# Performance work log

Measured on AMD Instinct MI355X. Metric: run time of the kernel, lower is better.

## Reference

```python
import jax, jax.numpy as jnp
import numpy as np

E = 8        # n_routed_experts
K = 2        # n_experts_per_token
H = 1024     # d_hidden
D = 512      # d_expert
NSH = 2      # n_shared_experts -> shared expert width = D*NSH


def setup_inputs() -> dict:
    key = jax.random.key(0)
    ks = jax.random.split(key, 8)
    s = 0.02
    x = jax.random.normal(ks[0], (4, 2048, H), jnp.float32)
    W_router = (jax.random.normal(ks[1], (H, E), jnp.float32) * s)
    Wg = (jax.random.normal(ks[2], (E, H, D), jnp.float32) * s)   # per-expert gate proj
    Wu = (jax.random.normal(ks[3], (E, H, D), jnp.float32) * s)   # per-expert up proj
    Wd = (jax.random.normal(ks[4], (E, D, H), jnp.float32) * s)   # per-expert down proj
    Ds = D * NSH
    Wsg = (jax.random.normal(ks[5], (H, Ds), jnp.float32) * s)
    Wsu = (jax.random.normal(ks[6], (H, Ds), jnp.float32) * s)
    Wsd = (jax.random.normal(ks[7], (Ds, H), jnp.float32) * s)
    return {"x": x, "W_router": W_router, "Wg": Wg, "Wu": Wu, "Wd": Wd,
            "Wsg": Wsg, "Wsu": Wsu, "Wsd": Wsd}


def reference(x, W_router, Wg, Wu, Wd, Wsg, Wsu, Wsd):
    B, S, Hd = x.shape
    T = B * S
    xf = x.reshape(T, Hd)

    # shared expert (SwiGLU)
    shared = (jax.nn.silu(xf @ Wsg) * (xf @ Wsu)) @ Wsd          # [T, H]

    # gating: softmax -> top-k -> renormalize
    logits = xf @ W_router                                        # [T, E]
    probs = jax.nn.softmax(logits, axis=-1)
    topk_scores, topk_idx = jax.lax.top_k(probs, K)               # [T, K]
    topk_scores = topk_scores / jnp.sum(topk_scores, axis=-1, keepdims=True)

    # combine weights: zero for unselected experts (topk indices are distinct,
    # so the original's first-match score selection equals a simple scatter)
    combine = jnp.zeros((T, E), x.dtype).at[jnp.arange(T)[:, None], topk_idx].set(topk_scores)

    # per-expert SwiGLU, computed densely and combined with sparse weights
    gate = jax.nn.silu(jnp.einsum('th,ehd->etd', xf, Wg))         # [E, T, D]
    up = jnp.einsum('th,ehd->etd', xf, Wu)                        # [E, T, D]
    expert_out = jnp.einsum('etd,edh->eth', gate * up, Wd)        # [E, T, H]
    routed = jnp.einsum('eth,te->th', expert_out, combine)        # [T, H]

    out = (routed + shared).reshape(B, S, Hd)

    # load-balancing aux loss: E * sum(mean_probs^2)
    probs_mean = jnp.mean(probs.reshape(B, S, E), axis=(0, 1))
    aux_loss = E * jnp.sum(probs_mean * probs_mean)
    return out, aux_loss
```

## Files before the change

### kernel.cpp

```cpp
#include <hip/hip_runtime.h>


typedef unsigned short u16;
typedef unsigned int   u32;
typedef short short8 __attribute__((ext_vector_type(8)));
typedef float f32x4  __attribute__((ext_vector_type(4)));

#define AS1 __attribute__((address_space(1)))
#define AS3 __attribute__((address_space(3)))

constexpr int T  = 8192;
constexpr int H  = 1024;
constexpr int E  = 8;
constexpr int D  = 512;
constexpr int DS = 1024;
constexpr int PAIR_CAP  = 18432;
constexpr int MT_ROUTED = 72;
constexpr int RB = 512;

constexpr int GU_ROUTED_BLKS = 4 * MT_ROUTED;
constexpr int GU_SHARED_BLKS = 8 * (T / 256);
constexpr int GU_BLKS  = GU_ROUTED_BLKS + GU_SHARED_BLKS;
constexpr int DNR_BLKS = 4 * MT_ROUTED;
constexpr int DNS_BLKS = 4 * (T / 256);
constexpr int DN_BLKS  = DNR_BLKS + DNS_BLKS;

__device__ __forceinline__ u16 f2bf(float f){
  u32 u = __builtin_bit_cast(u32, f);
  u += 0x7fffu + ((u >> 16) & 1u);
  return (u16)(u >> 16);
}
__device__ __forceinline__ float bf2f(u16 h){
  u32 u = ((u32)h) << 16;
  return __builtin_bit_cast(float, u);
}

__device__ __forceinline__ void gl_lds16(const u16* g, u16* l){
  __builtin_amdgcn_global_load_lds((const AS1 void*)g, (AS3 void*)l, 16, 0, 0);
}

template<int N>
__device__ __forceinline__ void wait_vm(){ __builtin_amdgcn_s_waitcnt(0x0f70 | N); }

__device__ __forceinline__ void bar_raw(){
  __builtin_amdgcn_s_barrier();
}
__device__ __forceinline__ void bar_pin(){
  __builtin_amdgcn_s_barrier();
  __builtin_amdgcn_sched_barrier(0);
}

__device__ __forceinline__ int swz_off(int c, int lane){
  return ((c ^ (lane & 7)) * 8);
}

template<int NWG>
__device__ __forceinline__ int xcd_tau(int fid){
  return (fid & 7) * (NWG >> 3) + (fid >> 3);
}

__global__ void __launch_bounds__(256) router_kernel(
    const float* __restrict__ x, const float* __restrict__ Wr,
    u16* __restrict__ xb,
    int* __restrict__ topk_idx, float* __restrict__ topk_w,
    int* __restrict__ partial_hist, float* __restrict__ partial_probs)
{
  __shared__ int   hist_s[4][8];
  __shared__ float ps_s[4][8];
  int tid = threadIdx.x, lane = tid & 63, wv = tid >> 6;
  int   histl[8] = {0,0,0,0,0,0,0,0};
  float psl[8]   = {0.f,0.f,0.f,0.f,0.f,0.f,0.f,0.f};

  for (int it = 0; it < 4; ++it){
    int t = blockIdx.x * 16 + wv * 4 + it;
    const float4* xr = (const float4*)(x + (long)t * H);
    uint2* xbr = (uint2*)(xb + (long)t * H);
    float acc[8];
#pragma unroll
    for (int e = 0; e < 8; ++e) acc[e] = 0.f;
#pragma unroll
    for (int i = 0; i < 4; ++i){
      float4 xv = xr[i * 64 + lane];
      u32 lo = (u32)f2bf(xv.x) | ((u32)f2bf(xv.y) << 16);
      u32 hi = (u32)f2bf(xv.z) | ((u32)f2bf(xv.w) << 16);
      xbr[i * 64 + lane] = make_uint2(lo, hi);
      int h0 = i * 256 + lane * 4;
#pragma unroll
      for (int j = 0; j < 4; ++j){
        float xs = (j == 0) ? xv.x : (j == 1) ? xv.y : (j == 2) ? xv.z : xv.w;
        const float4* wr = (const float4*)(Wr + (long)(h0 + j) * E);
        float4 w0 = wr[0], w1 = wr[1];
        acc[0] += xs * w0.x; acc[1] += xs * w0.y; acc[2] += xs * w0.z; acc[3] += xs * w0.w;
        acc[4] += xs * w1.x; acc[5] += xs * w1.y; acc[6] += xs * w1.z; acc[7] += xs * w1.w;
      }
    }
#pragma unroll
    for (int off = 32; off >= 1; off >>= 1){
#pragma unroll
      for (int e = 0; e < 8; ++e) acc[e] += __shfl_xor(acc[e], off, 64);
    }
    if (lane == 0){
      float m = acc[0];
#pragma unroll
      for (int e = 1; e < 8; ++e) m = fmaxf(m, acc[e]);
      float p[8], s = 0.f;
#pragma unroll
      for (int e = 0; e < 8; ++e){ p[e] = __expf(acc[e] - m); s += p[e]; }
      float inv = 1.f / s;
#pragma unroll
      for (int e = 0; e < 8; ++e) psl[e] += p[e] * inv;
      int i1 = 0; float v1 = p[0];
#pragma unroll
      for (int e = 1; e < 8; ++e) if (p[e] > v1){ v1 = p[e]; i1 = e; }
      int i2 = -1; float v2 = -1.f;
#pragma unroll
      for (int e = 0; e < 8; ++e) if (e != i1 && p[e] > v2){ v2 = p[e]; i2 = e; }
      float rs = 1.f / (v1 + v2);
      topk_idx[2 * t] = i1; topk_idx[2 * t + 1] = i2;
      topk_w[2 * t] = v1 * rs; topk_w[2 * t + 1] = v2 * rs;
      histl[i1]++; histl[i2]++;
    }
  }
  if (lane == 0){
#pragma unroll
    for (int e = 0; e < 8; ++e){ hist_s[wv][e] = histl[e]; ps_s[wv][e] = psl[e]; }
  }
  __syncthreads();
  if (tid < 8){
    int hs = 0; float ps = 0.f;
#pragma unroll
    for (int w = 0; w < 4; ++w){ hs += hist_s[w][tid]; ps += ps_s[w][tid]; }
    partial_hist[blockIdx.x * 8 + tid]  = hs;
    partial_probs[blockIdx.x * 8 + tid] = ps;
  }
}

__global__ void __launch_bounds__(64) scan_kernel(
    const int* __restrict__ partial_hist, const float* __restrict__ partial_probs,
    int* __restrict__ block_offset, float* __restrict__ out_aux,
    int* __restrict__ meta)
{
  __shared__ int   csum[8][8];
  __shared__ float cps[8][8];
  __shared__ int   cbase[8][8];
  __shared__ int   base_s[8];
  int tid = threadIdx.x, e = tid & 7, c = tid >> 3;
  int s = 0; float f = 0.f;
  for (int b = c * 64; b < c * 64 + 64; ++b){
    s += partial_hist[b * 8 + e]; f += partial_probs[b * 8 + e];
  }
  csum[c][e] = s; cps[c][e] = f;
  __syncthreads();
  if (tid < 8){
    int tot = 0;
    for (int cc = 0; cc < 8; ++cc){ cbase[cc][tid] = tot; tot += csum[cc][tid]; }
    csum[0][tid] = tot;
  }
  __syncthreads();
  if (tid == 0){
    int off = 0;
    for (int ee = 0; ee < 8; ++ee){ base_s[ee] = off; off += (csum[0][ee] + 255) & ~255; }
    meta[0] = off;
    float a = 0.f;
    for (int ee = 0; ee < 8; ++ee){
      float ps = 0.f;
      for (int cc = 0; cc < 8; ++cc) ps += cps[cc][ee];
      float m = ps * (1.f / (float)T);
      a += m * m;
    }
    out_aux[0] = (float)E * a;
  }
  __syncthreads();
  int run = base_s[e] + cbase[c][e];
  for (int b = c * 64; b < c * 64 + 64; ++b){
    block_offset[b * 8 + e] = run;
    run += partial_hist[b * 8 + e];
  }
}

__global__ void __launch_bounds__(64) scatter_kernel(
    const int* __restrict__ topk_idx, const float* __restrict__ topk_w,
    const int* __restrict__ block_offset,
    int* __restrict__ pair_token, int* __restrict__ pair_expert,
    float* __restrict__ pair_score, int* __restrict__ token_pos)
{
  int lane = threadIdx.x, b = blockIdx.x;
  if (lane >= 32) return;
  int idx = b * 32 + lane;
  int t = idx >> 1;
  int e = topk_idx[idx];
  float w = topk_w[idx];
  unsigned long long below = lane ? ((1ull << lane) - 1ull) : 0ull;
  int rank = 0, basee = 0;
#pragma unroll
  for (int ee = 0; ee < 8; ++ee){
    unsigned long long m = __ballot(e == ee);
    if (e == ee){ rank = __popcll(m & below); basee = block_offset[b * 8 + ee]; }
  }
  int pos = basee + rank;
  pair_token[pos] = t;
  pair_expert[pos] = e;
  pair_score[pos] = w;
  token_pos[idx] = pos;
}

__global__ void __launch_bounds__(256) transpose_all(
    const float* __restrict__ Wsg, const float* __restrict__ Wsu, u16* __restrict__ WsguT,
    const float* __restrict__ Wsd, u16* __restrict__ WsdT,
    const float* __restrict__ Wg,  const float* __restrict__ Wu, u16* __restrict__ WguT,
    const float* __restrict__ Wd,  u16* __restrict__ WdT)
{
  __shared__ float tile[32][33];
  int z = blockIdx.z;
  const float* src; u16* dst; int R, C, itype;
  if (z < 3){
    R = 1024; C = 1024;
    if (z == 0){ src = Wsg; dst = WsguT; itype = 1; }
    else if (z == 1){ src = Wsu; dst = WsguT; itype = 2; }
    else { src = Wsd; dst = WsdT; itype = 0; }
  } else if (z < 19){
    R = 1024; C = 512;
    int p = z - 3;
    if (p < 8){ src = Wg + (long)p * R * C; dst = WguT + (long)p * (2 * D * H); itype = 1; }
    else      { src = Wu + (long)(p - 8) * R * C; dst = WguT + (long)(p - 8) * (2 * D * H); itype = 2; }
  } else {
    R = 512; C = 1024;
    int p = z - 19;
    src = Wd + (long)p * R * C; dst = WdT + (long)p * R * C; itype = 0;
  }
  int tx = threadIdx.x & 31, ty = threadIdx.x >> 5;
  int c = blockIdx.x * 32 + tx;
  int rb = blockIdx.y * 32;
  if (blockIdx.x * 32 >= C || rb >= R) return;
#pragma unroll
  for (int j = 0; j < 4; ++j)
    tile[ty + j * 8][tx] = src[(long)(rb + ty + j * 8) * C + c];
  __syncthreads();
#pragma unroll
  for (int j = 0; j < 4; ++j){
    int cc = blockIdx.x * 32 + ty + j * 8;
    int dr = (itype == 0) ? cc : ((cc >> 4) * 32 + (cc & 15) + ((itype == 2) ? 16 : 0));
    dst[(long)dr * R + rb + tx] = f2bf(tile[tx][ty + j * 8]);
  }
}

struct HalfStage { const u16* p[2]; };

__device__ __forceinline__ void half_init(HalfStage& hs, const u16* __restrict__ gbase,
    int ld, int rowbase, const int* __restrict__ gather, int wave, int lane){
  int lr = lane >> 3, ch = lane & 7;
  int chs = (ch ^ lr) * 8;
#pragma unroll
  for (int j = 0; j < 2; ++j){
    int row = (wave * 2 + j) * 8 + lr;
    int grow = gather ? gather[rowbase + row] : (rowbase + row);
    hs.p[j] = gbase + (long)grow * ld + chs;
  }
}

__device__ __forceinline__ void half_issue(const HalfStage& hs, int k0,
                                           u16* __restrict__ lds, int wave){
#pragma unroll
  for (int j = 0; j < 2; ++j)
    gl_lds16(hs.p[j] + k0, lds + (wave * 2 + j) * 512);
}

template<int EPI>
__device__ __forceinline__ void gemm256(
    const u16* __restrict__ A, const u16* __restrict__ B, int K, int NT,
    const int* __restrict__ gather, int m0, int n0,
    u16* __restrict__ o_bf, int o_ld,
    const float* __restrict__ pair_score, float* __restrict__ out,
    u16* __restrict__ As, u16* __restrict__ Bs)
{
  int tid = threadIdx.x, lane = tid & 63, wave = tid >> 6;
  int wm = wave >> 2, wn = wave & 3;
  int rl = lane & 15, q = lane >> 4;

  HalfStage a0, a1, b0, b1;
  half_init(a0, A, K, m0,       gather, wave, lane);
  half_init(a1, A, K, m0 + 128, gather, wave, lane);
  half_init(b0, B, K, n0,       nullptr, wave, lane);
  half_init(b1, B, K, n0 + 128, nullptr, wave, lane);

  f32x4 acc[8][4];
#pragma unroll
  for (int i = 0; i < 8; ++i)
#pragma unroll
    for (int j = 0; j < 4; ++j)
#pragma unroll
      for (int r = 0; r < 4; ++r) acc[i][j][r] = 0.f;

  half_issue(b0, 0, Bs + 0 * 8192, wave);
  half_issue(b1, 0, Bs + 1 * 8192, wave);
  half_issue(a0, 0, As + 0 * 8192, wave);
  half_issue(a1, 0, As + 1 * 8192, wave);
  if (NT > 1){
    half_issue(b0, 64, Bs + 2 * 8192, wave);
    half_issue(b1, 64, Bs + 3 * 8192, wave);
    wait_vm<4>();
  } else {
    wait_vm<0>();
  }
  bar_pin();

  int bhalf = wn >> 1, brow0 = (wn & 1) * 64;

#pragma unroll 1
  for (int t = 0; t < NT; ++t){
    int buf = t & 1, nbuf = buf ^ 1;
    const u16* Abase = As + (buf * 2 + wm) * 8192;
    const u16* Bbase = Bs + (buf * 2 + bhalf) * 8192;
    short8 bfr[2][4];
#pragma unroll
    for (int qd = 0; qd < 4; ++qd){
      short8 afr[2][2];
#pragma unroll
      for (int ks = 0; ks < 2; ++ks){
        int off = swz_off(ks * 4 + q, lane);
#pragma unroll
        for (int m = 0; m < 2; ++m)
          afr[ks][m] = *(const short8*)(Abase + (qd * 32 + m * 16 + rl) * 64 + off);
        if (qd == 0){
#pragma unroll
          for (int n = 0; n < 4; ++n)
            bfr[ks][n] = *(const short8*)(Bbase + (brow0 + n * 16 + rl) * 64 + off);
        }
      }
      if (qd == 0 && t + 1 < NT) half_issue(a0, (t + 1) * 64, As + (nbuf * 2 + 0) * 8192, wave);
      if (qd == 1 && t + 1 < NT) half_issue(a1, (t + 1) * 64, As + (nbuf * 2 + 1) * 8192, wave);
      if (qd == 2 && t + 2 < NT) half_issue(b0, (t + 2) * 64, Bs + (buf * 2 + 0) * 8192, wave);
      if (qd == 3 && t + 2 < NT) half_issue(b1, (t + 2) * 64, Bs + (buf * 2 + 1) * 8192, wave);
      bar_raw();
      __builtin_amdgcn_s_setprio(1);
#pragma unroll
      for (int ks = 0; ks < 2; ++ks)
#pragma unroll
        for (int m = 0; m < 2; ++m)
#pragma unroll
          for (int n = 0; n < 4; ++n)
            acc[qd * 2 + m][n] = __builtin_amdgcn_mfma_f32_16x16x32_bf16(
                afr[ks][m], bfr[ks][n], acc[qd * 2 + m][n], 0, 0, 0);
      __builtin_amdgcn_s_setprio(0);
      if (qd == 3){
        if (t + 2 < NT) wait_vm<4>(); else wait_vm<0>();
        bar_pin();
      } else {
        bar_raw();
      }
    }
  }

  int row0 = m0 + wm * 128;
  if constexpr (EPI == 0){
    int hcol0 = (n0 >> 1) + wn * 32;
#pragma unroll
    for (int mt = 0; mt < 8; ++mt)
#pragma unroll
      for (int ntp = 0; ntp < 2; ++ntp)
#pragma unroll
        for (int r = 0; r < 4; ++r){
          int row = row0 + mt * 16 + q * 4 + r;
          int col = hcol0 + ntp * 16 + rl;
          float g = acc[mt][2 * ntp][r], u = acc[mt][2 * ntp + 1][r];
          float h = g / (1.f + __expf(-g)) * u;
          o_bf[(long)row * o_ld + col] = f2bf(h);
        }
  } else if constexpr (EPI == 1){
    int col0 = n0 + wn * 64;
#pragma unroll
    for (int mt = 0; mt < 8; ++mt)
#pragma unroll
      for (int r = 0; r < 4; ++r){
        int row = row0 + mt * 16 + q * 4 + r;
        float s = pair_score[row];
        long rbase = (long)row * H;
#pragma unroll
        for (int n = 0; n < 4; ++n){
          int col = col0 + n * 16 + rl;
          o_bf[rbase + col] = f2bf(s * acc[mt][n][r]);
        }
      }
  } else {
    int col0 = n0 + wn * 64;
#pragma unroll
    for (int mt = 0; mt < 8; ++mt)
#pragma unroll
      for (int r = 0; r < 4; ++r){
        int row = row0 + mt * 16 + q * 4 + r;
        long o = (long)row * H;
#pragma unroll
        for (int n = 0; n < 4; ++n){
          int col = col0 + n * 16 + rl;
          out[o + col] = acc[mt][n][r];
        }
      }
  }
}

__global__ void __launch_bounds__(512, 2) gateup_fused(
    const u16* __restrict__ xb, const u16* __restrict__ WguT, u16* __restrict__ hr,
    const u16* __restrict__ WsguT, u16* __restrict__ hs,
    const int* __restrict__ pair_token, const int* __restrict__ pair_expert,
    const int* __restrict__ meta)
{
  __shared__ u16 As[4 * 8192];
  __shared__ u16 Bs[4 * 8192];
  int tau = xcd_tau<GU_BLKS>(blockIdx.x);
  if (tau < GU_ROUTED_BLKS){
    int mtile = tau >> 2, ntile = tau & 3;
    int m0 = mtile * 256;
    if (m0 >= meta[0]) return;
    int e = pair_expert[m0];
    gemm256<0>(xb, WguT + (long)e * (2 * D * H), H, H / 64, pair_token,
               m0, ntile * 256, hr, D, nullptr, nullptr, As, Bs);
  } else {
    int sidx = tau - GU_ROUTED_BLKS;
    int mtile = sidx >> 3, ntile = sidx & 7;
    gemm256<0>(xb, WsguT, H, H / 64, nullptr,
               mtile * 256, ntile * 256, hs, DS, nullptr, nullptr, As, Bs);
  }
}

__global__ void __launch_bounds__(512, 2) down_fused(
    const u16* __restrict__ hr, const u16* __restrict__ WdT, u16* __restrict__ rout,
    const float* __restrict__ pair_score, const int* __restrict__ pair_expert,
    const int* __restrict__ meta,
    const u16* __restrict__ hs, const u16* __restrict__ WsdT,
    float* __restrict__ out)
{
  __shared__ u16 As[4 * 8192];
  __shared__ u16 Bs[4 * 8192];
  int tau = xcd_tau<DN_BLKS>(blockIdx.x);
  if (tau < DNR_BLKS){
    int mtile = tau >> 2, ntile = tau & 3;
    int m0 = mtile * 256;
    if (m0 >= meta[0]) return;
    int e = pair_expert[m0];
    gemm256<1>(hr, WdT + (long)e * (H * D), D, D / 64, nullptr,
               m0, ntile * 256, rout, H, pair_score, nullptr, As, Bs);
  } else {
    int sidx = tau - DNR_BLKS;
    int mtile = sidx >> 2, ntile = sidx & 3;
    gemm256<2>(hs, WsdT, DS, DS / 64, nullptr,
               mtile * 256, ntile * 256, nullptr, 0, nullptr, out, As, Bs);
  }
}

__global__ void __launch_bounds__(256) combine_kernel(
    float* __restrict__ out, const u16* __restrict__ rout,
    const int* __restrict__ token_pos)
{
  int tid = threadIdx.x, lane = tid & 63, wv = tid >> 6;
#pragma unroll
  for (int it = 0; it < 4; ++it){
    int t = blockIdx.x * 16 + wv * 4 + it;
    int p0 = token_pos[2 * t], p1 = token_pos[2 * t + 1];
    const uint2* r0 = (const uint2*)(rout + (long)p0 * H);
    const uint2* r1 = (const uint2*)(rout + (long)p1 * H);
    float4* o = (float4*)(out + (long)t * H);
#pragma unroll
    for (int i = 0; i < 4; ++i){
      uint2 a = r0[i * 64 + lane], b = r1[i * 64 + lane];
      float4 v = o[i * 64 + lane];
      v.x += bf2f((u16)(a.x & 0xffff)) + bf2f((u16)(b.x & 0xffff));
      v.y += bf2f((u16)(a.x >> 16))    + bf2f((u16)(b.x >> 16));
      v.z += bf2f((u16)(a.y & 0xffff)) + bf2f((u16)(b.y & 0xffff));
      v.w += bf2f((u16)(a.y >> 16))    + bf2f((u16)(b.y >> 16));
      o[i * 64 + lane] = v;
    }
  }
}

extern "C" void kernel_launch(void* const* d_in, const int* in_sizes, int n_in,
                              void* d_out, int out_size, void* d_ws, size_t ws_size,
                              hipStream_t stream)
{
  (void)in_sizes; (void)n_in; (void)out_size; (void)ws_size;
  const float* x   = (const float*)d_in[0];
  const float* Wr  = (const float*)d_in[1];
  const float* Wg  = (const float*)d_in[2];
  const float* Wu  = (const float*)d_in[3];
  const float* Wd  = (const float*)d_in[4];
  const float* Wsg = (const float*)d_in[5];
  const float* Wsu = (const float*)d_in[6];
  const float* Wsd = (const float*)d_in[7];
  float* out = (float*)d_out;

  char* ws = (char*)d_ws;
  size_t off = 0;
  auto alloc = [&](size_t bytes) -> void* {
    void* p = ws + off; off += (bytes + 255) & ~(size_t)255; return p;
  };
  u16* xb    = (u16*)alloc((size_t)T * H * 2);
  u16* WsguT = (u16*)alloc((size_t)2 * DS * H * 2);
  u16* WsdT  = (u16*)alloc((size_t)H * DS * 2);
  u16* WguT  = (u16*)alloc((size_t)E * 2 * D * H * 2);
  u16* WdT   = (u16*)alloc((size_t)E * H * D * 2);
  u16* hs    = (u16*)alloc((size_t)T * DS * 2);
  u16* hr    = (u16*)alloc((size_t)PAIR_CAP * D * 2);
  u16* rout  = (u16*)alloc((size_t)PAIR_CAP * H * 2);
  int*   topk_idx  = (int*)alloc((size_t)T * 2 * 4);
  float* topk_w    = (float*)alloc((size_t)T * 2 * 4);
  int*   token_pos = (int*)alloc((size_t)T * 2 * 4);
  int*   partial_hist  = (int*)alloc((size_t)RB * 8 * 4);
  float* partial_probs = (float*)alloc((size_t)RB * 8 * 4);
  int*   block_offset  = (int*)alloc((size_t)RB * 8 * 4);
  int*   meta          = (int*)alloc(256);
  char* zbase = ws + off;
  int*   pair_token  = (int*)alloc((size_t)PAIR_CAP * 4);
  int*   pair_expert = (int*)alloc((size_t)PAIR_CAP * 4);
  float* pair_score  = (float*)alloc((size_t)PAIR_CAP * 4);
  size_t zbytes = (size_t)((ws + off) - zbase);

  (void)hipMemsetAsync(zbase, 0, zbytes, stream);

  transpose_all<<<dim3(32, 32, 27), 256, 0, stream>>>(
      Wsg, Wsu, WsguT, Wsd, WsdT, Wg, Wu, WguT, Wd, WdT);

  router_kernel<<<RB, 256, 0, stream>>>(x, Wr, xb, topk_idx, topk_w,
                                        partial_hist, partial_probs);
  scan_kernel<<<1, 64, 0, stream>>>(partial_hist, partial_probs, block_offset,
                                    out + (size_t)T * H, meta);
  scatter_kernel<<<RB, 64, 0, stream>>>(topk_idx, topk_w, block_offset,
                                        pair_token, pair_expert, pair_score, token_pos);

  gateup_fused<<<GU_BLKS, 512, 0, stream>>>(
      xb, WguT, hr, WsguT, hs, pair_token, pair_expert, meta);

  down_fused<<<DN_BLKS, 512, 0, stream>>>(
      hr, WdT, rout, pair_score, pair_expert, meta, hs, WsdT, out);

  combine_kernel<<<T / 16, 256, 0, stream>>>(out, rout, token_pos);
}
```

Before: 367.1 us.

## Load B operand fragments directly from global memory, dropping B LDS staging

The GEMM no longer stages the weight (B) tile through shared memory. Each wave instead reads its B fragments straight from global memory into registers every k-step, which halves LDS use and removes the B prefetch pipeline. The cost is that B reads are no longer shared across the two M-waves and are not prefetched ahead, so global-load latency now sits on the critical path. That also forces a full vmcnt(0) wait each iteration, serialising the remaining A prefetch.

Measured after the change: 472.7 us. 28.8% more time.

```diff
diff --git a/kernel.cpp b/kernel.cpp
--- a/kernel.cpp
+++ b/kernel.cpp
@@ -271,17 +271,20 @@
     const int* __restrict__ gather, int m0, int n0,
     u16* __restrict__ o_bf, int o_ld,
     const float* __restrict__ pair_score, float* __restrict__ out,
-    u16* __restrict__ As, u16* __restrict__ Bs)
+    u16* __restrict__ As)
 {
   int tid = threadIdx.x, lane = tid & 63, wave = tid >> 6;
   int wm = wave >> 2, wn = wave & 3;
   int rl = lane & 15, q = lane >> 4;
 
-  HalfStage a0, a1, b0, b1;
+  HalfStage a0, a1;
   half_init(a0, A, K, m0,       gather, wave, lane);
   half_init(a1, A, K, m0 + 128, gather, wave, lane);
-  half_init(b0, B, K, n0,       nullptr, wave, lane);
-  half_init(b1, B, K, n0 + 128, nullptr, wave, lane);
+
+  const u16* bp[4];
+#pragma unroll
+  for (int n = 0; n < 4; ++n)
+    bp[n] = B + (long)(n0 + wn * 64 + n * 16 + rl) * K + q * 8;
 
   f32x4 acc[8][4];
 #pragma unroll
@@ -291,26 +294,15 @@
 #pragma unroll
       for (int r = 0; r < 4; ++r) acc[i][j][r] = 0.f;
 
-  half_issue(b0, 0, Bs + 0 * 8192, wave);
-  half_issue(b1, 0, Bs + 1 * 8192, wave);
   half_issue(a0, 0, As + 0 * 8192, wave);
   half_issue(a1, 0, As + 1 * 8192, wave);
-  if (NT > 1){
-    half_issue(b0, 64, Bs + 2 * 8192, wave);
-    half_issue(b1, 64, Bs + 3 * 8192, wave);
-    wait_vm<4>();
-  } else {
-    wait_vm<0>();
-  }
+  wait_vm<0>();
   bar_pin();
-
-  int bhalf = wn >> 1, brow0 = (wn & 1) * 64;
 
 #pragma unroll 1
   for (int t = 0; t < NT; ++t){
     int buf = t & 1, nbuf = buf ^ 1;
     const u16* Abase = As + (buf * 2 + wm) * 8192;
-    const u16* Bbase = Bs + (buf * 2 + bhalf) * 8192;
     short8 bfr[2][4];
 #pragma unroll
     for (int qd = 0; qd < 4; ++qd){
@@ -324,13 +316,11 @@
         if (qd == 0){
 #pragma unroll
           for (int n = 0; n < 4; ++n)
-            bfr[ks][n] = *(const short8*)(Bbase + (brow0 + n * 16 + rl) * 64 + off);
+            bfr[ks][n] = *(const short8*)(bp[n] + t * 64 + ks * 32);
         }
       }
       if (qd == 0 && t + 1 < NT) half_issue(a0, (t + 1) * 64, As + (nbuf * 2 + 0) * 8192, wave);
       if (qd == 1 && t + 1 < NT) half_issue(a1, (t + 1) * 64, As + (nbuf * 2 + 1) * 8192, wave);
-      if (qd == 2 && t + 2 < NT) half_issue(b0, (t + 2) * 64, Bs + (buf * 2 + 0) * 8192, wave);
-      if (qd == 3 && t + 2 < NT) half_issue(b1, (t + 2) * 64, Bs + (buf * 2 + 1) * 8192, wave);
       bar_raw();
       __builtin_amdgcn_s_setprio(1);
 #pragma unroll
@@ -343,7 +333,7 @@
                 afr[ks][m], bfr[ks][n], acc[qd * 2 + m][n], 0, 0, 0);
       __builtin_amdgcn_s_setprio(0);
       if (qd == 3){
-        if (t + 2 < NT) wait_vm<4>(); else wait_vm<0>();
+        wait_vm<0>();
         bar_pin();
       } else {
         bar_raw();
@@ -405,7 +395,6 @@
     const int* __restrict__ meta)
 {
   __shared__ u16 As[4 * 8192];
-  __shared__ u16 Bs[4 * 8192];
   int tau = xcd_tau<GU_BLKS>(blockIdx.x);
   if (tau < GU_ROUTED_BLKS){
     int mtile = tau >> 2, ntile = tau & 3;
@@ -413,12 +402,12 @@
     if (m0 >= meta[0]) return;
     int e = pair_expert[m0];
     gemm256<0>(xb, WguT + (long)e * (2 * D * H), H, H / 64, pair_token,
-               m0, ntile * 256, hr, D, nullptr, nullptr, As, Bs);
+               m0, ntile * 256, hr, D, nullptr, nullptr, As);
   } else {
     int sidx = tau - GU_ROUTED_BLKS;
     int mtile = sidx >> 3, ntile = sidx & 7;
     gemm256<0>(xb, WsguT, H, H / 64, nullptr,
-               mtile * 256, ntile * 256, hs, DS, nullptr, nullptr, As, Bs);
+               mtile * 256, ntile * 256, hs, DS, nullptr, nullptr, As);
   }
 }
 
@@ -430,7 +419,6 @@
     float* __restrict__ out)
 {
   __shared__ u16 As[4 * 8192];
-  __shared__ u16 Bs[4 * 8192];
   int tau = xcd_tau<DN_BLKS>(blockIdx.x);
   if (tau < DNR_BLKS){
     int mtile = tau >> 2, ntile = tau & 3;
@@ -438,12 +426,12 @@
     if (m0 >= meta[0]) return;
     int e = pair_expert[m0];
     gemm256<1>(hr, WdT + (long)e * (H * D), D, D / 64, nullptr,
-               m0, ntile * 256, rout, H, pair_score, nullptr, As, Bs);
+               m0, ntile * 256, rout, H, pair_score, nullptr, As);
   } else {
     int sidx = tau - DNR_BLKS;
     int mtile = sidx >> 2, ntile = sidx & 3;
     gemm256<2>(hs, WsdT, DS, DS / 64, nullptr,
-               mtile * 256, ntile * 256, nullptr, 0, nullptr, out, As, Bs);
+               mtile * 256, ntile * 256, nullptr, 0, nullptr, out, As);
   }
 }
 
```
